# Kernel optimization log

Measured on AMD Instinct MI355X. Metric: run time of the kernel, lower is better.

The kernel has to match this reference:

```python
import jax, jax.numpy as jnp
import numpy as np

NEG = 0.01  # LeakyReLU default slope
EPS = 1e-5  # InstanceNorm eps

def conv(x, w, b=None, pad=0, groups=1):
    y = jax.lax.conv_general_dilated(x, w, (1, 1), [(pad, pad), (pad, pad)],
                                     dimension_numbers=('NCHW', 'OIHW', 'NCHW'),
                                     feature_group_count=groups)
    if b is not None:
        y = y + b[None, :, None, None]
    return y

def inorm(x):
    m = jnp.mean(x, axis=(2, 3), keepdims=True)
    v = jnp.var(x, axis=(2, 3), keepdims=True)
    return (x - m) / jnp.sqrt(v + EPS)

def lrelu(x):
    return jax.nn.leaky_relu(x, NEG)

def maxpool2(x):
    return jax.lax.reduce_window(x, -jnp.inf, jax.lax.max, (1, 1, 2, 2), (1, 1, 2, 2), 'VALID')

def setup_inputs() -> dict:
    key = jax.random.key(0)
    ks = jax.random.split(key, 17)
    C = 64
    def w(k, shape, fan_in):
        return (jax.random.normal(k, shape, jnp.float32) * (1.0 / np.sqrt(fan_in)))
    return {
        'x': jax.random.normal(ks[0], (4, 3, 256, 256), jnp.float32),
        'w_proj': w(ks[1], (C, 3, 3, 3), 27), 'b_proj': jnp.zeros((C,), jnp.float32),
        'w_a1': w(ks[2], (C // 4, C, 1, 1), C), 'w_a2': w(ks[3], (C, C // 4, 1, 1), C // 4),
        'w_ref': w(ks[4], (C, 1, 3, 3), 9), 'b_ref': jnp.zeros((C,), jnp.float32),
        'w_fuse': w(ks[5], (C, C, 1, 1), C), 'b_fuse': jnp.zeros((C,), jnp.float32),
        'w_con': w(ks[6], (2 * C * 4, 1, 3, 3), 9),
        'w_u1': w(ks[7], (C, 2 * C * 4, 1, 1), 2 * C * 4), 'b_u1': jnp.zeros((C,), jnp.float32),
        'w_u2': w(ks[8], (C, C, 3, 3), 9 * C), 'b_u2': jnp.zeros((C,), jnp.float32),
        'w_sc': w(ks[9], (C, 2 * C, 1, 1), 2 * C), 'b_sc': jnp.zeros((C,), jnp.float32),
    }

def reference(x, w_proj, b_proj, w_a1, w_a2, w_ref, b_ref, w_fuse, b_fuse,
              w_con, w_u1, b_u1, w_u2, b_u2, w_sc, b_sc):
    xp = conv(x, w_proj, b_proj, pad=1)
    B, C, H, W = xp.shape
    # --- high branch: pywt wavedec2+waverec2 is perfect reconstruction (identity);
    #     torch code detaches -> stop_gradient on the reconstruction path
    xw = jax.lax.stop_gradient(xp)
    a = jnp.mean(xw, axis=(2, 3), keepdims=True)          # AdaptiveAvgPool2d(1)
    a = lrelu(conv(a, w_a1))
    a = jax.nn.sigmoid(conv(a, w_a2))
    xw = xw * a
    xw = conv(xw, w_ref, b_ref, pad=1, groups=C)          # depthwise refine
    xw = lrelu(inorm(xw))
    # --- low branch: FFT low-pass box filter
    f = jnp.fft.fftshift(jnp.fft.fft2(xp), axes=(-2, -1))
    hl = int(H * 0.3 // 2); wl = int(W * 0.3 // 2)
    hc, wc = H // 2, W // 2
    mask = jnp.zeros((H, W), bool).at[hc - hl:hc + hl, wc - wl:wc + wl].set(True)
    low = jnp.fft.ifft2(jnp.fft.ifftshift(f * mask, axes=(-2, -1))).real
    low = lrelu(inorm(conv(low, w_fuse, b_fuse)))
    # --- hypergraph construct / unwrap
    xc = jnp.concatenate([xw, low], axis=1)               # [B, 2C, H, W]
    h = conv(xc, w_con, pad=1, groups=2 * C)              # [B, 2C*k, H, W]
    u = lrelu(inorm(conv(h, w_u1, b_u1)))
    u = lrelu(inorm(conv(u, w_u2, b_u2, pad=1)))
    feat = u + conv(xc, w_sc, b_sc)
    pooled = maxpool2(feat)
    return feat, pooled
```

## Files before the change

kernel.cpp:

```cpp
#include <hip/hip_runtime.h>
#include <hip/hip_bf16.h>

#define WIDTH 256
#define HW 65536
#define IMG 16777216
#define NIMG 256
#define NSPLIT 16

typedef __attribute__((ext_vector_type(8))) short bf8v;
typedef __attribute__((ext_vector_type(4))) float f4v;

__device__ __forceinline__ float lrelu_f(float v){ return v > 0.f ? v : 0.01f*v; }
__device__ __forceinline__ unsigned short bf16u(float v){
    __hip_bfloat16 h = __float2bfloat16(v);
    return *(unsigned short*)&h;
}

__global__ __launch_bounds__(256) void k_statsf(const float* __restrict__ ps, float* __restrict__ st)
{
    const int img = threadIdx.x;
    const float* p = ps + blockIdx.x * (256 * NSPLIT * 2) + img * (NSPLIT * 2);
    float* o = st + blockIdx.x * 512;
    float S = 0.f, S2 = 0.f;
#pragma unroll
    for (int q = 0; q < NSPLIT; q++) { S += p[q * 2]; S2 += p[q * 2 + 1]; }
    const float m = S / 65536.f;
    const float var = S2 / 65536.f - m * m;
    o[img * 2]     = m;
    o[img * 2 + 1] = rsqrtf(var + 1e-5f);
}

__global__ __launch_bounds__(256) void k_attention(const float* __restrict__ ps0,
    const float* __restrict__ wa1, const float* __restrict__ wa2, float* __restrict__ a2o)
{
    __shared__ float means[256];
    __shared__ float a1s[64];
    const int tid = threadIdx.x;
    {
        const float* p = ps0 + tid * (NSPLIT * 2);
        float S = 0.f;
#pragma unroll
        for (int q = 0; q < NSPLIT; q++) S += p[q * 2];
        means[tid] = S * (1.f / 65536.f);
    }
    __syncthreads();
    if (tid < 64) {
        const int b = tid >> 4, o = tid & 15;
        float s = 0.f;
        for (int c = 0; c < 64; c++) s += wa1[o * 64 + c] * means[b * 64 + c];
        a1s[b * 16 + o] = lrelu_f(s);
    }
    __syncthreads();
    {
        const int b = tid >> 6, c = tid & 63;
        float s = 0.f;
#pragma unroll
        for (int o = 0; o < 16; o++) s += wa2[c * 16 + o] * a1s[b * 16 + o];
        a2o[tid] = 1.f / (1.f + expf(-s));
    }
}

__global__ __launch_bounds__(256, 3) void k_proj(const float* __restrict__ x,
    const float* __restrict__ wt, const float* __restrict__ bias,
    float* __restrict__ out, float* __restrict__ ps0)
{
    __shared__ float wl[3][9][32];
    const int tid = threadIdx.x;
    const int og = tid >> 5, xg = tid & 31;
    const int half = blockIdx.x & 1;
    const int y = (blockIdx.x >> 1) & 255;
    const int b = blockIdx.x >> 9;
    const int o_base = half * 32;
    const int o0l = og * 4;
    const int x0 = xg * 8;
    const int split = y & (NSPLIT - 1);

    for (int idx = tid; idx < 3 * 9 * 32; idx += 256) {
        const int o = idx & 31;
        const int rest = idx >> 5;
        const int pos = rest % 9, cc = rest / 9;
        wl[cc][pos][o] = wt[((o_base + o) * 3 + cc) * 9 + pos];
    }
    __syncthreads();

    float acc[4][8];
#pragma unroll
    for (int i = 0; i < 4; i++)
#pragma unroll
        for (int j = 0; j < 8; j++) acc[i][j] = 0.f;

#pragma unroll 2
    for (int cc = 0; cc < 3; cc++) {
        const float* src = x + ((size_t)b * 3 + cc) * HW;
#pragma unroll
        for (int dy = 0; dy < 3; dy++) {
            const int yy = y + dy - 1;
            float vv[10];
            if (yy >= 0 && yy < 256) {
                const float* r = src + (size_t)yy * WIDTH;
                vv[0] = (x0 > 0) ? r[x0 - 1] : 0.f;
                const float4 m0 = *(const float4*)(r + x0);
                const float4 m1 = *(const float4*)(r + x0 + 4);
                vv[1] = m0.x; vv[2] = m0.y; vv[3] = m0.z; vv[4] = m0.w;
                vv[5] = m1.x; vv[6] = m1.y; vv[7] = m1.z; vv[8] = m1.w;
                vv[9] = (x0 < 248) ? r[x0 + 8] : 0.f;
            } else {
#pragma unroll
                for (int q = 0; q < 10; q++) vv[q] = 0.f;
            }
#pragma unroll
            for (int dx = 0; dx < 3; dx++) {
                const float4 w4 = *(const float4*)&wl[cc][dy * 3 + dx][o0l];
                const float wv[4] = { w4.x, w4.y, w4.z, w4.w };
#pragma unroll
                for (int oi = 0; oi < 4; oi++)
#pragma unroll
                    for (int px = 0; px < 8; px++)
                        acc[oi][px] += wv[oi] * vv[px + dx];
            }
        }
    }
#pragma unroll
    for (int oi = 0; oi < 4; oi++) {
        const int o = o_base + o0l + oi;
        const float bv = bias[o];
        const size_t off = ((size_t)(b * 64 + o)) * HW + (size_t)y * WIDTH + x0;
        float4 r0, r1;
        r0.x = acc[oi][0] + bv; r0.y = acc[oi][1] + bv; r0.z = acc[oi][2] + bv; r0.w = acc[oi][3] + bv;
        r1.x = acc[oi][4] + bv; r1.y = acc[oi][5] + bv; r1.z = acc[oi][6] + bv; r1.w = acc[oi][7] + bv;
        *(float4*)(out + off) = r0;
        *(float4*)(out + off + 4) = r1;
        float s  = r0.x + r0.y + r0.z + r0.w + r1.x + r1.y + r1.z + r1.w;
        float s2 = r0.x*r0.x + r0.y*r0.y + r0.z*r0.z + r0.w*r0.w
                 + r1.x*r1.x + r1.y*r1.y + r1.z*r1.z + r1.w*r1.w;
#pragma unroll
        for (int offt = 16; offt > 0; offt >>= 1) {
            s  += __shfl_down(s, offt, 32);
            s2 += __shfl_down(s2, offt, 32);
        }
        if (xg == 0) {
            float* pp = &ps0[((b * 64 + o) * NSPLIT + split) * 2];
            atomicAdd(pp, s);
            atomicAdd(pp + 1, s2);
        }
    }
}

__global__ __launch_bounds__(256) void k_dw(const float* __restrict__ xp, const float* __restrict__ a2,
    const float* __restrict__ wref, const float* __restrict__ bref, float* __restrict__ out,
    float* __restrict__ ps1)
{
    const int tid = threadIdx.x;
    const int img = blockIdx.x >> 6;
    const int y = ((blockIdx.x & 63) << 2) + (tid >> 6);
    const int x0 = (tid & 63) * 4;
    const int c = img & 63;
    const int split = blockIdx.x & (NSPLIT - 1);
    const float* src = xp + (size_t)img * HW;
    float wv[9];
#pragma unroll
    for (int k = 0; k < 9; k++) wv[k] = wref[c * 9 + k];
    const float scale = a2[img], bb = bref[c];

    float a[4] = {0.f, 0.f, 0.f, 0.f};
#pragma unroll
    for (int dy = 0; dy < 3; dy++) {
        const int yy = y + dy - 1;
        if (yy < 0 || yy > 255) continue;
        const float* r = src + (size_t)yy * WIDTH;
        float vv[6];
        vv[0] = (x0 > 0) ? r[x0 - 1] : 0.f;
        const float4 m = *(const float4*)(r + x0);
        vv[1] = m.x; vv[2] = m.y; vv[3] = m.z; vv[4] = m.w;
        vv[5] = (x0 < 252) ? r[x0 + 4] : 0.f;
#pragma unroll
        for (int dx = 0; dx < 3; dx++)
#pragma unroll
            for (int px = 0; px < 4; px++)
                a[px] += wv[dy * 3 + dx] * vv[px + dx];
    }
    float4 o;
    o.x = bb + scale * a[0]; o.y = bb + scale * a[1];
    o.z = bb + scale * a[2]; o.w = bb + scale * a[3];
    *(float4*)(out + (size_t)img * HW + (size_t)y * WIDTH + x0) = o;

    float s  = o.x + o.y + o.z + o.w;
    float s2 = o.x*o.x + o.y*o.y + o.z*o.z + o.w*o.w;
#pragma unroll
    for (int offt = 32; offt > 0; offt >>= 1) {
        s  += __shfl_down(s, offt, 64);
        s2 += __shfl_down(s2, offt, 64);
    }
    __shared__ float ls[4][2];
    const int wid = tid >> 6, lane = tid & 63;
    if (lane == 0) { ls[wid][0] = s; ls[wid][1] = s2; }
    __syncthreads();
    if (tid == 0) {
        const float S  = ls[0][0] + ls[1][0] + ls[2][0] + ls[3][0];
        const float S2 = ls[0][1] + ls[1][1] + ls[2][1] + ls[3][1];
        float* pp = &ps1[(img * NSPLIT + split) * 2];
        atomicAdd(pp, S);
        atomicAdd(pp + 1, S2);
    }
}

__global__ void k_tables(float* __restrict__ kr2, float* __restrict__ ki2)
{
    const int t = blockIdx.x * 256 + threadIdx.x;
    if (t < 512) {
        const int tm = t & 255;
        const double PI = 3.14159265358979323846;
        const double th = 2.0 * PI * (double)tm / 256.0;
        double sr = 1.0;
        for (int k = 1; k <= 37; k++) sr += 2.0 * cos((double)k * th);
        sr += cos(38.0 * th);
        kr2[t] = (float)(sr / 256.0);
        ki2[t] = (float)(-sin(38.0 * th) / 256.0);
    }
}

__global__ __launch_bounds__(256) void k_kmat(const float* __restrict__ kr2, const float* __restrict__ ki2,
    unsigned short* __restrict__ KBr, unsigned short* __restrict__ KBi)
{
    const int n = blockIdx.x, k = threadIdx.x;
    const int d = (n - k) & 255;
    KBr[n * 256 + k] = bf16u(kr2[d]);
    KBi[n * 256 + k] = bf16u(ki2[d]);
}

__global__ __launch_bounds__(256, 2) void k_mdft1(const float* __restrict__ xp,
    const unsigned short* __restrict__ KBr, const unsigned short* __restrict__ KBi,
    unsigned short* __restrict__ TR, unsigned short* __restrict__ TI)
{
    const int tid = threadIdx.x, lane = tid & 63, wave = tid >> 6;
    const int img = blockIdx.x >> 2;
    const int mb = (blockIdx.x >> 1) & 1, nb = blockIdx.x & 1;
    const int M0 = mb * 128 + (wave >> 1) * 64;
    const int N0 = nb * 128 + (wave & 1) * 64;
    const int lrow = lane & 15, lk = lane >> 4;
    const float* Xb = xp + (size_t)img * HW;

    f4v aR[4][4], aI[4][4];
#pragma unroll
    for (int m = 0; m < 4; m++)
#pragma unroll
        for (int n = 0; n < 4; n++) { aR[m][n] = (f4v){0,0,0,0}; aI[m][n] = (f4v){0,0,0,0}; }

#pragma unroll 1
    for (int k0 = 0; k0 < 256; k0 += 32) {
        bf8v af[4];
#pragma unroll
        for (int m = 0; m < 4; m++) {
            const float* rp = Xb + (size_t)(M0 + m * 16 + lrow) * 256 + k0 + lk * 8;
            const float4 a0 = *(const float4*)rp;
            const float4 a1 = *(const float4*)(rp + 4);
            bf8v t;
            t[0] = (short)bf16u(a0.x); t[1] = (short)bf16u(a0.y);
            t[2] = (short)bf16u(a0.z); t[3] = (short)bf16u(a0.w);
            t[4] = (short)bf16u(a1.x); t[5] = (short)bf16u(a1.y);
            t[6] = (short)bf16u(a1.z); t[7] = (short)bf16u(a1.w);
            af[m] = t;
        }
#pragma unroll
        for (int n = 0; n < 4; n++) {
            const int xcol = N0 + n * 16 + lrow;
            const bf8v br = *(const bf8v*)(KBr + xcol * 256 + k0 + lk * 8);
            const bf8v bi = *(const bf8v*)(KBi + xcol * 256 + k0 + lk * 8);
#pragma unroll
            for (int m = 0; m < 4; m++) {
                aR[m][n] = __builtin_amdgcn_mfma_f32_16x16x32_bf16(af[m], br, aR[m][n], 0, 0, 0);
                aI[m][n] = __builtin_amdgcn_mfma_f32_16x16x32_bf16(af[m], bi, aI[m][n], 0, 0, 0);
            }
        }
    }
#pragma unroll
    for (int n = 0; n < 4; n++) {
        const size_t xoff = (size_t)img * HW + (size_t)(N0 + n * 16 + lrow) * 256;
#pragma unroll
        for (int m = 0; m < 4; m++) {
            const size_t off = xoff + M0 + m * 16 + lk * 4;
            const f4v r = aR[m][n], ii = aI[m][n];
            ushort4 ur, ui;
            ur.x = bf16u(r[0]); ur.y = bf16u(r[1]); ur.z = bf16u(r[2]); ur.w = bf16u(r[3]);
            ui.x = bf16u(ii[0]); ui.y = bf16u(ii[1]); ui.z = bf16u(ii[2]); ui.w = bf16u(ii[3]);
            *(ushort4*)(TR + off) = ur;
            *(ushort4*)(TI + off) = ui;
        }
    }
}

__global__ __launch_bounds__(256, 2) void k_mdft2(const unsigned short* __restrict__ TR,
    const unsigned short* __restrict__ TI, const unsigned short* __restrict__ KBr,
    const unsigned short* __restrict__ KBi, float* __restrict__ low)
{
    const int tid = threadIdx.x, lane = tid & 63, wave = tid >> 6;
    const int img = blockIdx.x >> 2;
    const int mb = (blockIdx.x >> 1) & 1, nb = blockIdx.x & 1;
    const int M0 = mb * 128 + (wave >> 1) * 64;
    const int N0 = nb * 128 + (wave & 1) * 64;
    const int lrow = lane & 15, lk = lane >> 4;
    const unsigned short* TRb = TR + (size_t)img * HW;
    const unsigned short* TIb = TI + (size_t)img * HW;

    f4v aR[4][4], aI[4][4];
#pragma unroll
    for (int m = 0; m < 4; m++)
#pragma unroll
        for (int n = 0; n < 4; n++) { aR[m][n] = (f4v){0,0,0,0}; aI[m][n] = (f4v){0,0,0,0}; }

#pragma unroll 1
    for (int k0 = 0; k0 < 256; k0 += 32) {
        bf8v afR[4], afI[4];
#pragma unroll
        for (int m = 0; m < 4; m++) {
            const int ro = (M0 + m * 16 + lrow) * 256 + k0 + lk * 8;
            afR[m] = *(const bf8v*)(TRb + ro);
            afI[m] = *(const bf8v*)(TIb + ro);
        }
#pragma unroll
        for (int n = 0; n < 4; n++) {
            const int ycol = N0 + n * 16 + lrow;
            const bf8v br = *(const bf8v*)(KBr + ycol * 256 + k0 + lk * 8);
            const bf8v bi = *(const bf8v*)(KBi + ycol * 256 + k0 + lk * 8);
#pragma unroll
            for (int m = 0; m < 4; m++) {
                aR[m][n] = __builtin_amdgcn_mfma_f32_16x16x32_bf16(afR[m], br, aR[m][n], 0, 0, 0);
                aI[m][n] = __builtin_amdgcn_mfma_f32_16x16x32_bf16(afI[m], bi, aI[m][n], 0, 0, 0);
            }
        }
    }
#pragma unroll
    for (int n = 0; n < 4; n++) {
        const size_t yoff = (size_t)img * HW + (size_t)(N0 + n * 16 + lrow) * 256;
#pragma unroll
        for (int m = 0; m < 4; m++) {
            const f4v r = aR[m][n], ii = aI[m][n];
            const float4 v = make_float4(r[0] - ii[0], r[1] - ii[1], r[2] - ii[2], r[3] - ii[3]);
            *(float4*)(low + yoff + M0 + m * 16 + lk * 4) = v;
        }
    }
}

__global__ __launch_bounds__(256) void k_weff_bf(const float* __restrict__ w_u1,
    const float* __restrict__ w_con, unsigned short* __restrict__ wbf)
{
    const int f = blockIdx.x * 256 + threadIdx.x;
    if (f >= 73728) return;
    const int ch = f & 31, oc = (f >> 5) & 63, cp = f >> 11;
    const int pos = cp % 9, cb = cp / 9;
    const int g = cb * 32 + ch;
    float s = 0.f;
#pragma unroll
    for (int j = 0; j < 4; j++) s += w_u1[oc * 512 + g * 4 + j] * w_con[(g * 4 + j) * 9 + pos];
    wbf[f] = bf16u(s);
}

template<int CIN>
__global__ __launch_bounds__(256) void k_wcvt(const float* __restrict__ w, unsigned short* __restrict__ wbf)
{
    const int f = blockIdx.x * 256 + threadIdx.x;
    if (f >= 64 * CIN * 9) return;
    const int ch = f & 31, oc = (f >> 5) & 63, cp = f >> 11;
    const int pos = cp % 9, cb = cp / 9;
    const int c = cb * 32 + ch;
    wbf[f] = bf16u(w[oc * CIN * 9 + c * 9 + pos]);
}

template<int CIN>
__global__ __launch_bounds__(256) void k_wcvt1(const float* __restrict__ w, unsigned short* __restrict__ wbf)
{
    const int f = blockIdx.x * 256 + threadIdx.x;
    if (f >= 64 * CIN) return;
    const int ch = f & 31, oc = (f >> 5) & 63, cb = f >> 11;
    wbf[f] = bf16u(w[oc * CIN + cb * 32 + ch]);
}

template<int CIN>
__global__ __launch_bounds__(512, 4) void k_mconv(
    const float* __restrict__ in0, const float* __restrict__ in1,
    const unsigned short* __restrict__ wbf, const float* __restrict__ bias,
    float* __restrict__ out,
    const float* __restrict__ stA, const float* __restrict__ stB,
    float* __restrict__ psOut)
{
    __shared__ unsigned short Xl[4 * 260 * 32];
    __shared__ float sh_ms[2 * CIN];
    __shared__ float red[8][64][2];
    const int tid = threadIdx.x;
    const int lane = tid & 63;
    const int wave = tid >> 6;
    const int b = blockIdx.x >> 7;
    const int y0 = (blockIdx.x & 127) * 2;
    const int row_sel = wave & 1;
    const int px_base = (wave >> 1) * 64;
    const int split = blockIdx.x & (NSPLIT - 1);

    for (int i = tid; i < 4 * 260 * 32 / 2; i += 512) ((unsigned int*)Xl)[i] = 0u;
    for (int j = tid; j < 2 * CIN; j += 512) {
        const int cg = j >> 1;
        const float* st = (CIN == 128 && cg >= 64) ? stB : stA;
        sh_ms[j] = st[(b * 64 + (cg & 63)) * 2 + (j & 1)];
    }

    f4v acc[4][4];
#pragma unroll
    for (int i = 0; i < 4; i++)
#pragma unroll
        for (int n = 0; n < 4; n++) acc[i][n] = (f4v){0.f, 0.f, 0.f, 0.f};

    const int lrow = lane & 15;
    const int gsl  = lane >> 4;
    const int wlane = lrow * 32 + gsl * 8;

    __syncthreads();

    constexpr int NC = CIN / 32;
#pragma unroll 1
    for (int cb = 0; cb < NC; cb++) {
        const int c0 = cb * 32;
        const bool second = (CIN == 128 && c0 >= 64);
        const float* src = (second ? in1 : in0) + ((size_t)b * 64 + (c0 & 63)) * HW;
        const float* ms = sh_ms + cb * 64;
        {
            const int q   = tid & 63;
            const int g   = (tid >> 6) & 3;
            const int rg  = tid >> 8;
            const int px0 = q * 4;
#pragma unroll
            for (int r2 = 0; r2 < 2; r2++) {
                const int r = rg * 2 + r2;
                const int yy = y0 - 1 + r;
                if (yy < 0 || yy > 255) continue;
                const float* rp = src + (size_t)(g * 8) * HW + (size_t)yy * WIDTH + px0;
                float v[8][4];
#pragma unroll
                for (int cc = 0; cc < 8; cc++) {
                    const float4 ld = *(const float4*)(rp + (size_t)cc * HW);
                    const float mm  = ms[(g * 8 + cc) * 2];
                    const float ssv = ms[(g * 8 + cc) * 2 + 1];
                    v[cc][0] = lrelu_f((ld.x - mm) * ssv);
                    v[cc][1] = lrelu_f((ld.y - mm) * ssv);
                    v[cc][2] = lrelu_f((ld.z - mm) * ssv);
                    v[cc][3] = lrelu_f((ld.w - mm) * ssv);
                }
#pragma unroll
                for (int p = 0; p < 4; p++) {
                    const int slot = px0 + p + 1;
                    const int sw = (slot >> 1) & 3;
                    uint4 w4;
                    w4.x = (unsigned)bf16u(v[0][p]) | ((unsigned)bf16u(v[1][p]) << 16);
                    w4.y = (unsigned)bf16u(v[2][p]) | ((unsigned)bf16u(v[3][p]) << 16);
                    w4.z = (unsigned)bf16u(v[4][p]) | ((unsigned)bf16u(v[5][p]) << 16);
                    w4.w = (unsigned)bf16u(v[6][p]) | ((unsigned)bf16u(v[7][p]) << 16);
                    *(uint4*)((char*)Xl + r * 16640 + slot * 64 + ((g ^ sw) << 4)) = w4;
                }
            }
        }
        __syncthreads();
#pragma unroll 1
        for (int pos = 0; pos < 9; pos++) {
            const int dy = pos / 3, dx = pos - dy * 3;
            const unsigned short* wp = wbf + (cb * 9 + pos) * 2048 + wlane;
            const bf8v wf0 = *(const bf8v*)(wp);
            const bf8v wf1 = *(const bf8v*)(wp + 512);
            const bf8v wf2 = *(const bf8v*)(wp + 1024);
            const bf8v wf3 = *(const bf8v*)(wp + 1536);
            const int pxe = px_base + lrow + dx;
            const int row = row_sel + dy;
            const char* abase = (const char*)Xl + row * 16640 + pxe * 64
                              + ((gsl ^ ((pxe >> 1) & 3)) << 4);
#pragma unroll
            for (int i = 0; i < 4; i++) {
                const bf8v af = *(const bf8v*)(abase + i * 1024);
                acc[i][0] = __builtin_amdgcn_mfma_f32_16x16x32_bf16(af, wf0, acc[i][0], 0, 0, 0);
                acc[i][1] = __builtin_amdgcn_mfma_f32_16x16x32_bf16(af, wf1, acc[i][1], 0, 0, 0);
                acc[i][2] = __builtin_amdgcn_mfma_f32_16x16x32_bf16(af, wf2, acc[i][2], 0, 0, 0);
                acc[i][3] = __builtin_amdgcn_mfma_f32_16x16x32_bf16(af, wf3, acc[i][3], 0, 0, 0);
            }
        }
        __syncthreads();
    }
    const int yrow = y0 + row_sel;
    const int lk = gsl;
#pragma unroll
    for (int n = 0; n < 4; n++) {
        const float bv = bias[n * 16 + lrow];
        float* po = out + ((size_t)(b * 64) + n * 16 + lrow) * HW
                  + (size_t)yrow * WIDTH + px_base + lk * 4;
        float s = 0.f, s2 = 0.f;
#pragma unroll
        for (int i = 0; i < 4; i++) {
            const f4v a = acc[i][n];
            float4 v;
            v.x = a[0] + bv; v.y = a[1] + bv; v.z = a[2] + bv; v.w = a[3] + bv;
            s  += v.x + v.y + v.z + v.w;
            s2 += v.x*v.x + v.y*v.y + v.z*v.z + v.w*v.w;
            *(float4*)(po + i * 16) = v;
        }
        s  += __shfl_down(s, 32);  s  += __shfl_down(s, 16);
        s2 += __shfl_down(s2, 32); s2 += __shfl_down(s2, 16);
        if (lk == 0) { red[wave][n * 16 + lrow][0] = s; red[wave][n * 16 + lrow][1] = s2; }
    }
    __syncthreads();
    if (tid < 64) {
        float S = 0.f, S2 = 0.f;
#pragma unroll
        for (int w = 0; w < 8; w++) { S += red[w][tid][0]; S2 += red[w][tid][1]; }
        float* pp = &psOut[((b * 64 + tid) * NSPLIT + split) * 2];
        atomicAdd(pp, S);
        atomicAdd(pp + 1, S2);
    }
}

template<int CIN, bool ADD, bool NORMIN, bool STATS>
__global__ __launch_bounds__(256, 3) void k_pconv(
    const float* __restrict__ in0, const float* __restrict__ in1,
    const unsigned short* __restrict__ wbf, const float* __restrict__ bias,
    const float* __restrict__ addsrc, float* __restrict__ out,
    const float* __restrict__ stA, const float* __restrict__ stB,
    const float* __restrict__ stAdd, float* __restrict__ psOut)
{
    __shared__ unsigned short Xl[256 * 32];
    __shared__ float sh_ms[2 * CIN];
    __shared__ float red[4][64][2];
    const int tid = threadIdx.x, lane = tid & 63, wave = tid >> 6;
    const int y = blockIdx.x & 255, b = blockIdx.x >> 8;
    const int split = blockIdx.x & (NSPLIT - 1);
    const int lrow = lane & 15, gsl = lane >> 4;
    const int wpx = wave * 64;
    const int wlane = lrow * 32 + gsl * 8;

    if constexpr (NORMIN) {
        for (int j = tid; j < 2 * CIN; j += 256) {
            const int cg = j >> 1;
            const float* st = (CIN == 128 && cg >= 64) ? stB : stA;
            sh_ms[j] = st[(b * 64 + (cg & 63)) * 2 + (j & 1)];
        }
    }

    f4v acc[4][4];
#pragma unroll
    for (int m = 0; m < 4; m++)
#pragma unroll
        for (int n = 0; n < 4; n++) acc[m][n] = (f4v){0.f, 0.f, 0.f, 0.f};

    __syncthreads();

    constexpr int NC = CIN / 32;
#pragma unroll 1
    for (int cb = 0; cb < NC; cb++) {
        const int c0 = cb * 32;
        const bool second = (CIN == 128 && c0 >= 64);
        const float* src = (second ? in1 : in0) + ((size_t)b * 64 + (c0 & 63)) * HW
                         + (size_t)y * WIDTH;
        const float* ms = sh_ms + cb * 64;
        {
            const int q = tid & 63, g = tid >> 6;
            const int px0 = q * 4;
            const float* rp = src + (size_t)(g * 8) * HW + px0;
            float v[8][4];
#pragma unroll
            for (int cc = 0; cc < 8; cc++) {
                const float4 ld = *(const float4*)(rp + (size_t)cc * HW);
                if constexpr (NORMIN) {
                    const float mm  = ms[(g * 8 + cc) * 2];
                    const float ssv = ms[(g * 8 + cc) * 2 + 1];
                    v[cc][0] = lrelu_f((ld.x - mm) * ssv);
                    v[cc][1] = lrelu_f((ld.y - mm) * ssv);
                    v[cc][2] = lrelu_f((ld.z - mm) * ssv);
                    v[cc][3] = lrelu_f((ld.w - mm) * ssv);
                } else {
                    v[cc][0] = ld.x; v[cc][1] = ld.y; v[cc][2] = ld.z; v[cc][3] = ld.w;
                }
            }
#pragma unroll
            for (int p = 0; p < 4; p++) {
                const int px = px0 + p;
                const int sw = (px >> 1) & 3;
                uint4 w4;
                w4.x = (unsigned)bf16u(v[0][p]) | ((unsigned)bf16u(v[1][p]) << 16);
                w4.y = (unsigned)bf16u(v[2][p]) | ((unsigned)bf16u(v[3][p]) << 16);
                w4.z = (unsigned)bf16u(v[4][p]) | ((unsigned)bf16u(v[5][p]) << 16);
                w4.w = (unsigned)bf16u(v[6][p]) | ((unsigned)bf16u(v[7][p]) << 16);
                *(uint4*)((char*)Xl + px * 64 + ((g ^ sw) << 4)) = w4;
            }
        }
        __syncthreads();
        {
            const unsigned short* wp = wbf + cb * 2048 + wlane;
            const bf8v wf0 = *(const bf8v*)(wp);
            const bf8v wf1 = *(const bf8v*)(wp + 512);
            const bf8v wf2 = *(const bf8v*)(wp + 1024);
            const bf8v wf3 = *(const bf8v*)(wp + 1536);
#pragma unroll
            for (int m = 0; m < 4; m++) {
                const int px = wpx + m * 16 + lrow;
                const char* abase = (const char*)Xl + px * 64
                                  + ((gsl ^ ((px >> 1) & 3)) << 4);
                const bf8v af = *(const bf8v*)abase;
                acc[m][0] = __builtin_amdgcn_mfma_f32_16x16x32_bf16(af, wf0, acc[m][0], 0, 0, 0);
                acc[m][1] = __builtin_amdgcn_mfma_f32_16x16x32_bf16(af, wf1, acc[m][1], 0, 0, 0);
                acc[m][2] = __builtin_amdgcn_mfma_f32_16x16x32_bf16(af, wf2, acc[m][2], 0, 0, 0);
                acc[m][3] = __builtin_amdgcn_mfma_f32_16x16x32_bf16(af, wf3, acc[m][3], 0, 0, 0);
            }
        }
        __syncthreads();
    }
    const int lk = gsl;
#pragma unroll
    for (int n = 0; n < 4; n++) {
        const int oc = n * 16 + lrow;
        const float bv = bias[oc];
        float mm = 0.f, ss = 0.f;
        if constexpr (ADD) { mm = stAdd[(b * 64 + oc) * 2]; ss = stAdd[(b * 64 + oc) * 2 + 1]; }
        const size_t orow = ((size_t)(b * 64 + oc)) * HW + (size_t)y * WIDTH;
        float s = 0.f, s2 = 0.f;
#pragma unroll
        for (int m = 0; m < 4; m++) {
            const int px = wpx + m * 16 + lk * 4;
            const f4v a = acc[m][n];
            float r[4] = { a[0] + bv, a[1] + bv, a[2] + bv, a[3] + bv };
            if constexpr (ADD) {
                const float4 av = *(const float4*)(addsrc + orow + px);
                r[0] += lrelu_f((av.x - mm) * ss);
                r[1] += lrelu_f((av.y - mm) * ss);
                r[2] += lrelu_f((av.z - mm) * ss);
                r[3] += lrelu_f((av.w - mm) * ss);
            }
            *(float4*)(out + orow + px) = make_float4(r[0], r[1], r[2], r[3]);
            if constexpr (STATS) {
                s  += r[0] + r[1] + r[2] + r[3];
                s2 += r[0]*r[0] + r[1]*r[1] + r[2]*r[2] + r[3]*r[3];
            }
        }
        if constexpr (STATS) {
            s  += __shfl_down(s, 32);  s  += __shfl_down(s, 16);
            s2 += __shfl_down(s2, 32); s2 += __shfl_down(s2, 16);
            if (lk == 0) { red[wave][oc][0] = s; red[wave][oc][1] = s2; }
        }
    }
    if constexpr (STATS) {
        __syncthreads();
        if (tid < 64) {
            const float S  = red[0][tid][0] + red[1][tid][0] + red[2][tid][0] + red[3][tid][0];
            const float S2 = red[0][tid][1] + red[1][tid][1] + red[2][tid][1] + red[3][tid][1];
            float* pp = &psOut[((b * 64 + tid) * NSPLIT + split) * 2];
            atomicAdd(pp, S);
            atomicAdd(pp + 1, S2);
        }
    }
}

__global__ __launch_bounds__(256) void k_maxpool(const float* __restrict__ feat, float* __restrict__ out)
{
    const int idx = blockIdx.x * 256 + threadIdx.x;
    const int xo = idx & 127;
    const int yo = (idx >> 7) & 127;
    const int img = idx >> 14;
    const float* p = feat + (size_t)img * HW + (size_t)(yo * 2) * WIDTH + xo * 2;
    out[idx] = fmaxf(fmaxf(p[0], p[1]), fmaxf(p[WIDTH], p[WIDTH + 1]));
}

extern "C" void kernel_launch(void* const* d_in, const int* in_sizes, int n_in,
                              void* d_out, int out_size, void* d_ws, size_t ws_size,
                              hipStream_t stream)
{
    const float* x      = (const float*)d_in[0];
    const float* w_proj = (const float*)d_in[1];
    const float* b_proj = (const float*)d_in[2];
    const float* w_a1   = (const float*)d_in[3];
    const float* w_a2   = (const float*)d_in[4];
    const float* w_ref  = (const float*)d_in[5];
    const float* b_ref  = (const float*)d_in[6];
    const float* w_fuse = (const float*)d_in[7];
    const float* b_fuse = (const float*)d_in[8];
    const float* w_con  = (const float*)d_in[9];
    const float* w_u1   = (const float*)d_in[10];
    const float* b_u1   = (const float*)d_in[11];
    const float* w_u2   = (const float*)d_in[12];
    const float* b_u2   = (const float*)d_in[13];
    const float* w_sc   = (const float*)d_in[14];
    const float* b_sc   = (const float*)d_in[15];

    float* wsf  = (float*)d_ws;
    float* buf0 = wsf;
    float* buf1 = wsf + (size_t)IMG;
    float* buf2 = wsf + (size_t)2 * IMG;
    float* aux  = wsf + (size_t)3 * IMG;
    float* a2b  = aux;
    float* kr2  = aux + 256;
    float* ki2  = aux + 768;
    unsigned short* wbfA = (unsigned short*)(aux + 1280);
    unsigned short* wbfB = wbfA + 73728;
    unsigned short* KBr  = wbfB + 36864;
    unsigned short* KBi  = KBr + 65536;
    unsigned short* wbfF = KBi + 65536;
    unsigned short* wbfS = wbfF + 4096;
    float* ps   = aux + 1280 + 120832 + 6144;
    float* st   = ps + 5 * 256 * NSPLIT * 2;

    float* fout = (float*)d_out;
    float* pout = fout + (size_t)IMG;
    unsigned short* T1R = (unsigned short*)buf2;
    unsigned short* T1I = T1R + (size_t)IMG;

    const int PSSLOT = 256 * NSPLIT * 2;

    hipMemsetAsync(ps, 0, 5 * PSSLOT * sizeof(float), stream);
    k_tables<<<2, 256, 0, stream>>>(kr2, ki2);
    k_kmat<<<256, 256, 0, stream>>>(kr2, ki2, KBr, KBi);
    k_weff_bf<<<288, 256, 0, stream>>>(w_u1, w_con, wbfA);
    k_wcvt<64><<<144, 256, 0, stream>>>(w_u2, wbfB);
    k_wcvt1<64><<<16, 256, 0, stream>>>(w_fuse, wbfF);
    k_wcvt1<128><<<32, 256, 0, stream>>>(w_sc, wbfS);
    k_proj<<<2048, 256, 0, stream>>>(x, w_proj, b_proj, buf0, ps);
    k_attention<<<1, 256, 0, stream>>>(ps, w_a1, w_a2, a2b);
    k_dw<<<16384, 256, 0, stream>>>(buf0, a2b, w_ref, b_ref, buf1, ps + PSSLOT);
    k_mdft1<<<1024, 256, 0, stream>>>(buf0, KBr, KBi, T1R, T1I);
    k_mdft2<<<1024, 256, 0, stream>>>(T1R, T1I, KBr, KBi, fout);
    k_pconv<64, false, false, true><<<1024, 256, 0, stream>>>(
        fout, nullptr, wbfF, b_fuse, nullptr, buf0,
        nullptr, nullptr, nullptr, ps + 2 * PSSLOT);
    k_statsf<<<2, 256, 0, stream>>>(ps + PSSLOT, st + 512);
    k_mconv<128><<<512, 512, 0, stream>>>(buf1, buf0, wbfA, b_u1, fout,
        st + 512, st + 1024, ps + 3 * PSSLOT);
    k_statsf<<<1, 256, 0, stream>>>(ps + 3 * PSSLOT, st + 1536);
    k_mconv<64><<<512, 512, 0, stream>>>(fout, nullptr, wbfB, b_u2, buf2,
        st + 1536, st + 1536, ps + 4 * PSSLOT);
    k_statsf<<<1, 256, 0, stream>>>(ps + 4 * PSSLOT, st + 2048);
    k_pconv<128, true, true, false><<<1024, 256, 0, stream>>>(
        buf1, buf0, wbfS, b_sc, buf2, fout,
        st + 512, st + 1024, st + 2048, nullptr);
    k_maxpool<<<16384, 256, 0, stream>>>(fout, pout);
}
```

Before: 531.7 us.

## Fuse maxpool into final shortcut pconv and split staging loads to cut registers

Replaces the final k_pconv<128> plus separate k_maxpool with a new k_pconv2 kernel. Each block handles a pair of rows, computes the shortcut 1x1 conv with MFMA, adds the normalized residual, writes feat, then re-reads its own two rows to produce the pooled output. This removes one launch and a full pass over feat for pooling. Separately, the mconv staging loop is split into two halves of four channels to lower live register pressure. The pooling re-read depends on global writes within the block becoming visible after __syncthreads.

```diff
diff --git a/kernel.cpp b/kernel.cpp
--- a/kernel.cpp
+++ b/kernel.cpp
@@ -432,27 +432,48 @@
                 const int yy = y0 - 1 + r;
                 if (yy < 0 || yy > 255) continue;
                 const float* rp = src + (size_t)(g * 8) * HW + (size_t)yy * WIDTH + px0;
-                float v[8][4];
-#pragma unroll
-                for (int cc = 0; cc < 8; cc++) {
-                    const float4 ld = *(const float4*)(rp + (size_t)cc * HW);
-                    const float mm  = ms[(g * 8 + cc) * 2];
-                    const float ssv = ms[(g * 8 + cc) * 2 + 1];
-                    v[cc][0] = lrelu_f((ld.x - mm) * ssv);
-                    v[cc][1] = lrelu_f((ld.y - mm) * ssv);
-                    v[cc][2] = lrelu_f((ld.z - mm) * ssv);
-                    v[cc][3] = lrelu_f((ld.w - mm) * ssv);
+                uint2 pk[4];
+                {
+                    float v[4][4];
+#pragma unroll
+                    for (int cc = 0; cc < 4; cc++) {
+                        const float4 ld = *(const float4*)(rp + (size_t)cc * HW);
+                        const float mm  = ms[(g * 8 + cc) * 2];
+                        const float ssv = ms[(g * 8 + cc) * 2 + 1];
+                        v[cc][0] = lrelu_f((ld.x - mm) * ssv);
+                        v[cc][1] = lrelu_f((ld.y - mm) * ssv);
+                        v[cc][2] = lrelu_f((ld.z - mm) * ssv);
+                        v[cc][3] = lrelu_f((ld.w - mm) * ssv);
+                    }
+#pragma unroll
+                    for (int p = 0; p < 4; p++) {
+                        pk[p].x = (unsigned)bf16u(v[0][p]) | ((unsigned)bf16u(v[1][p]) << 16);
+                        pk[p].y = (unsigned)bf16u(v[2][p]) | ((unsigned)bf16u(v[3][p]) << 16);
+                    }
                 }
-#pragma unroll
-                for (int p = 0; p < 4; p++) {
-                    const int slot = px0 + p + 1;
-                    const int sw = (slot >> 1) & 3;
-                    uint4 w4;
-                    w4.x = (unsigned)bf16u(v[0][p]) | ((unsigned)bf16u(v[1][p]) << 16);
-                    w4.y = (unsigned)bf16u(v[2][p]) | ((unsigned)bf16u(v[3][p]) << 16);
-                    w4.z = (unsigned)bf16u(v[4][p]) | ((unsigned)bf16u(v[5][p]) << 16);
-                    w4.w = (unsigned)bf16u(v[6][p]) | ((unsigned)bf16u(v[7][p]) << 16);
-                    *(uint4*)((char*)Xl + r * 16640 + slot * 64 + ((g ^ sw) << 4)) = w4;
+                {
+                    float v[4][4];
+#pragma unroll
+                    for (int cc = 0; cc < 4; cc++) {
+                        const float4 ld = *(const float4*)(rp + (size_t)(4 + cc) * HW);
+                        const float mm  = ms[(g * 8 + 4 + cc) * 2];
+                        const float ssv = ms[(g * 8 + 4 + cc) * 2 + 1];
+                        v[cc][0] = lrelu_f((ld.x - mm) * ssv);
+                        v[cc][1] = lrelu_f((ld.y - mm) * ssv);
+                        v[cc][2] = lrelu_f((ld.z - mm) * ssv);
+                        v[cc][3] = lrelu_f((ld.w - mm) * ssv);
+                    }
+#pragma unroll
+                    for (int p = 0; p < 4; p++) {
+                        const int slot = px0 + p + 1;
+                        const int sw = (slot >> 1) & 3;
+                        uint4 w4;
+                        w4.x = pk[p].x;
+                        w4.y = pk[p].y;
+                        w4.z = (unsigned)bf16u(v[0][p]) | ((unsigned)bf16u(v[1][p]) << 16);
+                        w4.w = (unsigned)bf16u(v[2][p]) | ((unsigned)bf16u(v[3][p]) << 16);
+                        *(uint4*)((char*)Xl + r * 16640 + slot * 64 + ((g ^ sw) << 4)) = w4;
+                    }
                 }
             }
         }
@@ -651,14 +672,142 @@
     }
 }
 
-__global__ __launch_bounds__(256) void k_maxpool(const float* __restrict__ feat, float* __restrict__ out)
-{
-    const int idx = blockIdx.x * 256 + threadIdx.x;
-    const int xo = idx & 127;
-    const int yo = (idx >> 7) & 127;
-    const int img = idx >> 14;
-    const float* p = feat + (size_t)img * HW + (size_t)(yo * 2) * WIDTH + xo * 2;
-    out[idx] = fmaxf(fmaxf(p[0], p[1]), fmaxf(p[WIDTH], p[WIDTH + 1]));
+__global__ __launch_bounds__(512, 4) void k_pconv2(
+    const float* __restrict__ in0, const float* __restrict__ in1,
+    const unsigned short* __restrict__ wbf, const float* __restrict__ bias,
+    const float* __restrict__ addsrc, float* __restrict__ out, float* __restrict__ pout,
+    const float* __restrict__ stA, const float* __restrict__ stB,
+    const float* __restrict__ stAdd)
+{
+    __shared__ unsigned short Xl[2][256 * 32];
+    __shared__ float sh_ms[2 * 128];
+    const int tid = threadIdx.x, lane = tid & 63, wave = tid >> 6;
+    const int b = blockIdx.x >> 7;
+    const int Y = blockIdx.x & 127;
+    const int row_sel = wave & 1;
+    const int wpx = (wave >> 1) * 64;
+    const int lrow = lane & 15, gsl = lane >> 4;
+    const int wlane = lrow * 32 + gsl * 8;
+    const int y = 2 * Y + row_sel;
+
+    for (int j = tid; j < 256; j += 512) {
+        const int cg = j >> 1;
+        const float* st = (cg >= 64) ? stB : stA;
+        sh_ms[j] = st[(b * 64 + (cg & 63)) * 2 + (j & 1)];
+    }
+
+    f4v acc[4][4];
+#pragma unroll
+    for (int m = 0; m < 4; m++)
+#pragma unroll
+        for (int n = 0; n < 4; n++) acc[m][n] = (f4v){0.f, 0.f, 0.f, 0.f};
+
+    __syncthreads();
+
+#pragma unroll 1
+    for (int cb = 0; cb < 4; cb++) {
+        const int c0 = cb * 32;
+        const bool second = (c0 >= 64);
+        const float* src = (second ? in1 : in0) + ((size_t)b * 64 + (c0 & 63)) * HW;
+        const float* ms = sh_ms + cb * 64;
+        {
+            const int q = tid & 63, g = (tid >> 6) & 3, rg = tid >> 8;
+            const int px0 = q * 4;
+            const int yy = 2 * Y + rg;
+            const float* rp = src + (size_t)(g * 8) * HW + (size_t)yy * WIDTH + px0;
+            uint2 pk[4];
+            {
+                float v[4][4];
+#pragma unroll
+                for (int cc = 0; cc < 4; cc++) {
+                    const float4 ld = *(const float4*)(rp + (size_t)cc * HW);
+                    const float mm  = ms[(g * 8 + cc) * 2];
+                    const float ssv = ms[(g * 8 + cc) * 2 + 1];
+                    v[cc][0] = lrelu_f((ld.x - mm) * ssv);
+                    v[cc][1] = lrelu_f((ld.y - mm) * ssv);
+                    v[cc][2] = lrelu_f((ld.z - mm) * ssv);
+                    v[cc][3] = lrelu_f((ld.w - mm) * ssv);
+                }
+#pragma unroll
+                for (int p = 0; p < 4; p++) {
+                    pk[p].x = (unsigned)bf16u(v[0][p]) | ((unsigned)bf16u(v[1][p]) << 16);
+                    pk[p].y = (unsigned)bf16u(v[2][p]) | ((unsigned)bf16u(v[3][p]) << 16);
+                }
+            }
+            {
+                float v[4][4];
+#pragma unroll
+                for (int cc = 0; cc < 4; cc++) {
+                    const float4 ld = *(const float4*)(rp + (size_t)(4 + cc) * HW);
+                    const float mm  = ms[(g * 8 + 4 + cc) * 2];
+                    const float ssv = ms[(g * 8 + 4 + cc) * 2 + 1];
+                    v[cc][0] = lrelu_f((ld.x - mm) * ssv);
+                    v[cc][1] = lrelu_f((ld.y - mm) * ssv);
+                    v[cc][2] = lrelu_f((ld.z - mm) * ssv);
+                    v[cc][3] = lrelu_f((ld.w - mm) * ssv);
+                }
+#pragma unroll
+                for (int p = 0; p < 4; p++) {
+                    const int px = px0 + p;
+                    const int sw = (px >> 1) & 3;
+                    uint4 w4;
+                    w4.x = pk[p].x;
+                    w4.y = pk[p].y;
+                    w4.z = (unsigned)bf16u(v[0][p]) | ((unsigned)bf16u(v[1][p]) << 16);
+                    w4.w = (unsigned)bf16u(v[2][p]) | ((unsigned)bf16u(v[3][p]) << 16);
+                    *(uint4*)((char*)Xl[rg] + px * 64 + ((g ^ sw) << 4)) = w4;
+                }
+            }
+        }
+        __syncthreads();
+        {
+            const unsigned short* wp = wbf + cb * 2048 + wlane;
+            const bf8v wf0 = *(const bf8v*)(wp);
+            const bf8v wf1 = *(const bf8v*)(wp + 512);
+            const bf8v wf2 = *(const bf8v*)(wp + 1024);
+            const bf8v wf3 = *(const bf8v*)(wp + 1536);
+#pragma unroll
+            for (int m = 0; m < 4; m++) {
+                const int px = wpx + m * 16 + lrow;
+                const char* abase = (const char*)Xl[row_sel] + px * 64
+                                  + ((gsl ^ ((px >> 1) & 3)) << 4);
+                const bf8v af = *(const bf8v*)abase;
+                acc[m][0] = __builtin_amdgcn_mfma_f32_16x16x32_bf16(af, wf0, acc[m][0], 0, 0, 0);
+                acc[m][1] = __builtin_amdgcn_mfma_f32_16x16x32_bf16(af, wf1, acc[m][1], 0, 0, 0);
+                acc[m][2] = __builtin_amdgcn_mfma_f32_16x16x32_bf16(af, wf2, acc[m][2], 0, 0, 0);
+                acc[m][3] = __builtin_amdgcn_mfma_f32_16x16x32_bf16(af, wf3, acc[m][3], 0, 0, 0);
+            }
+        }
+        __syncthreads();
+    }
+#pragma unroll
+    for (int n = 0; n < 4; n++) {
+        const int oc = n * 16 + lrow;
+        const float bv = bias[oc];
+        const float mm = stAdd[(b * 64 + oc) * 2], ss = stAdd[(b * 64 + oc) * 2 + 1];
+        const size_t orow = ((size_t)(b * 64 + oc)) * HW + (size_t)y * WIDTH;
+#pragma unroll
+        for (int m = 0; m < 4; m++) {
+            const int px = wpx + m * 16 + gsl * 4;
+            const f4v a = acc[m][n];
+            float r[4] = { a[0] + bv, a[1] + bv, a[2] + bv, a[3] + bv };
+            const float4 av = *(const float4*)(addsrc + orow + px);
+            r[0] += lrelu_f((av.x - mm) * ss);
+            r[1] += lrelu_f((av.y - mm) * ss);
+            r[2] += lrelu_f((av.z - mm) * ss);
+            r[3] += lrelu_f((av.w - mm) * ss);
+            *(float4*)(out + orow + px) = make_float4(r[0], r[1], r[2], r[3]);
+        }
+    }
+    __syncthreads();
+    for (int e = tid; e < 64 * 128; e += 512) {
+        const int xo = e & 127, oc = e >> 7;
+        const float* f0 = out + ((size_t)(b * 64 + oc)) * HW + (size_t)(2 * Y) * WIDTH + 2 * xo;
+        const float2 a = *(const float2*)f0;
+        const float2 c = *(const float2*)(f0 + WIDTH);
+        pout[((size_t)(b * 64 + oc)) * (HW / 4) + Y * 128 + xo]
+            = fmaxf(fmaxf(a.x, a.y), fmaxf(c.x, c.y));
+    }
 }
 
 extern "C" void kernel_launch(void* const* d_in, const int* in_sizes, int n_in,
@@ -728,8 +877,7 @@
     k_mconv<64><<<512, 512, 0, stream>>>(fout, nullptr, wbfB, b_u2, buf2,
         st + 1536, st + 1536, ps + 4 * PSSLOT);
     k_statsf<<<1, 256, 0, stream>>>(ps + 4 * PSSLOT, st + 2048);
-    k_pconv<128, true, true, false><<<1024, 256, 0, stream>>>(
-        buf1, buf0, wbfS, b_sc, buf2, fout,
-        st + 512, st + 1024, st + 2048, nullptr);
-    k_maxpool<<<16384, 256, 0, stream>>>(fout, pout);
-}
+    k_pconv2<<<512, 512, 0, stream>>>(
+        buf1, buf0, wbfS, b_sc, buf2, fout, pout,
+        st + 512, st + 1024, st + 2048);
+}
```

After: 532.2 us. About the same (+0.1%).
